# Kernel tuning notes

Hardware: AMD Instinct MI355X
Metric: run time of the kernel (lower is better)

Reference implementation:

```python
import jax, jax.numpy as jnp
import numpy as np

EPS = 1e-5

def weight_quant(w):
    # Per-tensor 1.58-bit quantization: scale by 1/mean(|w|), round (half-to-even,
    # matching torch.round), clamp to {-1,0,1}.
    scale = 1.0 / jnp.clip(jnp.mean(jnp.abs(w)), EPS, None)
    return jnp.clip(jnp.round(w * scale), -1.0, 1.0)

def setup_inputs() -> dict:
    key = jax.random.key(0)
    k1, k2, k3 = jax.random.split(key, 3)
    O, I, B = 4096, 4096, 4096
    V = jax.random.normal(k1, (O, I), dtype=jnp.float32)
    # V_p is a quantized (ternary) version of a weight matrix, as in BitNet-style PTQ
    V_p = weight_quant(jax.random.normal(k2, (O, I), dtype=jnp.float32))
    X = jax.random.normal(k3, (B, I), dtype=jnp.float32)
    theta = jnp.float32(0.2)
    bias = jnp.float32(0.0)
    return {"V": V, "V_p": V_p, "X": X, "theta": theta, "bias": bias}

def reference(V, V_p, X, theta, bias):
    cos_t = jnp.cos(theta)
    # Residual direction T, then ternarize it
    T = (V - V_p * cos_t) / jnp.sin(theta)
    Tq = weight_quant(T)                       # [O, I] in {-1,0,1}
    X_T = jnp.matmul(X, Tq.T)                  # [B, O]
    V_p_X = jnp.matmul(X, V_p.T)               # [B, O]
    sign = jax.lax.stop_gradient(jnp.sign(X_T * 100.0))
    appx = cos_t * V_p_X + sign * bias
    return appx
```

## Files before the change

### kernel.cpp

```cpp
#include <hip/hip_runtime.h>

#define EPSQ 1e-5f

typedef signed char i8;
using int4v = __attribute__((ext_vector_type(4))) int;

constexpr int DIM = 4096;

__device__ __forceinline__ void gload_lds16(const void* g, void* l) {
  __builtin_amdgcn_global_load_lds(
      (const __attribute__((address_space(1))) void*)(g),
      (__attribute__((address_space(3))) void*)(l), 16, 0, 0);
}

__global__ __launch_bounds__(256)
void k_prep(const float* __restrict__ X, const float* __restrict__ V,
            const float* __restrict__ Vp,
            const float* __restrict__ theta_p, const float* __restrict__ bias_p,
            i8* __restrict__ Xq, float* __restrict__ rs,
            i8* __restrict__ W1, float* __restrict__ partial) {
  __shared__ float wred[4];
  const int tid = threadIdx.x;
  const int b = blockIdx.x;
  if (b < 4096) {
    const int row = b;
    const float4* Xr = (const float4*)(X + (size_t)row * DIM);
    float4 f[4];
    float mx = 0.0f;
    #pragma unroll
    for (int t = 0; t < 4; ++t) {
      f[t] = Xr[tid + t * 256];
      mx = fmaxf(mx, fmaxf(fmaxf(fabsf(f[t].x), fabsf(f[t].y)),
                           fmaxf(fabsf(f[t].z), fabsf(f[t].w))));
    }
    #pragma unroll
    for (int off = 32; off > 0; off >>= 1) mx = fmaxf(mx, __shfl_down(mx, off, 64));
    int lane = tid & 63, w = tid >> 6;
    if (lane == 0) wred[w] = mx;
    __syncthreads();
    mx = fmaxf(fmaxf(wred[0], wred[1]), fmaxf(wred[2], wred[3]));
    mx = fmaxf(mx, 1e-30f);
    float rsv = mx / 127.0f;
    if (tid == 0) rs[row] = rsv;
    float inv = 1.0f / rsv;
    char4* Xo = (char4*)(Xq + (size_t)row * DIM);
    #pragma unroll
    for (int t = 0; t < 4; ++t) {
      char4 qv;
      qv.x = (i8)fminf(fmaxf(rintf(f[t].x * inv), -127.0f), 127.0f);
      qv.y = (i8)fminf(fmaxf(rintf(f[t].y * inv), -127.0f), 127.0f);
      qv.z = (i8)fminf(fmaxf(rintf(f[t].z * inv), -127.0f), 127.0f);
      qv.w = (i8)fminf(fmaxf(rintf(f[t].w * inv), -127.0f), 127.0f);
      Xo[tid + t * 256] = qv;
    }
  } else if (b < 6144) {
    const float4* Vp4 = (const float4*)Vp;
    char4* W1o = (char4*)W1;
    const int total4 = DIM * DIM / 4;
    const int stride = 2048 * 256;
    for (int i = (b - 4096) * 256 + tid; i < total4; i += stride) {
      float4 vp = Vp4[i];
      char4 w1;
      w1.x = (i8)vp.x; w1.y = (i8)vp.y; w1.z = (i8)vp.z; w1.w = (i8)vp.w;
      W1o[i] = w1;
    }
  } else {
    if (bias_p[0] == 0.0f) return;
    float ct = cosf(theta_p[0]);
    float st = sinf(theta_p[0]);
    const float4* V4  = (const float4*)V;
    const float4* Vp4 = (const float4*)Vp;
    float acc = 0.0f;
    const int total4 = DIM * DIM / 4;
    const int stride = 2048 * 256;
    for (int i = (b - 6144) * 256 + tid; i < total4; i += stride) {
      float4 v = V4[i], vp = Vp4[i];
      acc += fabsf((v.x - vp.x * ct) / st) + fabsf((v.y - vp.y * ct) / st)
           + fabsf((v.z - vp.z * ct) / st) + fabsf((v.w - vp.w * ct) / st);
    }
    #pragma unroll
    for (int off = 32; off > 0; off >>= 1) acc += __shfl_down(acc, off, 64);
    int lane = tid & 63, w = tid >> 6;
    if (lane == 0) wred[w] = acc;
    __syncthreads();
    if (tid == 0) partial[b - 6144] = wred[0] + wred[1] + wred[2] + wred[3];
  }
}

__global__ __launch_bounds__(256)
void k_quantT(const float* __restrict__ V, const float* __restrict__ Vp,
              const float* __restrict__ theta_p, const float* __restrict__ bias_p,
              const float* __restrict__ partial, i8* __restrict__ W2) {
  if (bias_p[0] == 0.0f) return;
  __shared__ float wred[4];
  __shared__ float stot;
  const int tid = threadIdx.x;
  float s = 0.0f;
  #pragma unroll
  for (int i = 0; i < 8; ++i) s += partial[tid + i * 256];
  #pragma unroll
  for (int off = 32; off > 0; off >>= 1) s += __shfl_down(s, off, 64);
  int lane = tid & 63, w = tid >> 6;
  if (lane == 0) wred[w] = s;
  __syncthreads();
  if (tid == 0) stot = wred[0] + wred[1] + wred[2] + wred[3];
  __syncthreads();
  float mean = fmaxf(stot / 16777216.0f, EPSQ);
  float scale = 1.0f / mean;
  float ctv = cosf(theta_p[0]);
  float stv = sinf(theta_p[0]);
  const float4* V4  = (const float4*)V;
  const float4* Vp4 = (const float4*)Vp;
  char4* W2o = (char4*)W2;
  const int total4 = DIM * DIM / 4;
  const int stride = 2048 * 256;
  for (int i = blockIdx.x * 256 + tid; i < total4; i += stride) {
    float4 v = V4[i], vp = Vp4[i];
    char4 w2;
    w2.x = (i8)fminf(fmaxf(rintf(((v.x - vp.x * ctv) / stv) * scale), -1.0f), 1.0f);
    w2.y = (i8)fminf(fmaxf(rintf(((v.y - vp.y * ctv) / stv) * scale), -1.0f), 1.0f);
    w2.z = (i8)fminf(fmaxf(rintf(((v.z - vp.z * ctv) / stv) * scale), -1.0f), 1.0f);
    w2.w = (i8)fminf(fmaxf(rintf(((v.w - vp.w * ctv) / stv) * scale), -1.0f), 1.0f);
    W2o[i] = w2;
  }
}

__global__ __launch_bounds__(512, 2)
void k_gemm(const i8* __restrict__ A, const i8* __restrict__ B1,
            const i8* __restrict__ B2, float* __restrict__ C,
            const float* __restrict__ rs, const float* __restrict__ theta_p,
            const float* __restrict__ bias_p) {
  __shared__ i8 sm[131072];

  const int tid  = threadIdx.x;
  const int lane = tid & 63;
  const int w    = tid >> 6;
  const int l15  = lane & 15;
  const int kq   = lane >> 4;
  const int wm   = (w >> 2) * 128;
  const int wn   = (w & 3) * 64;
  const int bm   = blockIdx.y * 256;
  const int bn   = blockIdx.x * 256;

  int offg[4];
  #pragma unroll
  for (int ln = 0; ln < 4; ++ln) {
    int p = ln * 512 + tid;
    int r = p >> 3;
    int c = (p & 7) ^ (r & 7);
    offg[ln] = r * DIM + c * 16;
  }

  const int swz0 = ((0 * 4 + kq) ^ (l15 & 7)) * 16;
  const int swz1 = ((1 * 4 + kq) ^ (l15 & 7)) * 16;
  const int arow = (wm + l15) * 128;
  const int brow = (wn + l15) * 128;

  const float biasv = bias_p[0];
  const int npass = (biasv != 0.0f) ? 2 : 1;
  const float ct = cosf(theta_p[0]);

  for (int pass = 0; pass < npass; ++pass) {
    const bool signp = (npass == 2 && pass == 0);
    const i8* Ag = A + (size_t)bm * DIM;
    const i8* Bg = (signp ? B2 : B1) + (size_t)bn * DIM;

    int4v acc[8][4] = {};

    #pragma unroll
    for (int ln = 0; ln < 4; ++ln) {
      const int sb = (ln * 512 + w * 64) * 16;
      gload_lds16(Ag + offg[ln], sm + sb);
      gload_lds16(Bg + offg[ln], sm + 32768 + sb);
    }
    asm volatile("s_waitcnt vmcnt(0)" ::: "memory");
    __builtin_amdgcn_s_barrier();

    #pragma unroll 2
    for (int t = 0; t < 32; ++t) {
      const i8* As = sm + (t & 1) * 65536;
      const i8* Bs = As + 32768;
      i8* Asta = sm + ((t + 1) & 1) * 65536;
      i8* Bsta = Asta + 32768;
      const bool dostage = (t + 1 < 32);
      const int ktn = (t + 1) * 128;

      int4v af[4][2], bf[2][2];
      #pragma unroll
      for (int q = 0; q < 4; ++q) {
        const int mh = q >> 1, nh = q & 1;
        if (nh == 0) {
          #pragma unroll
          for (int i4 = 0; i4 < 4; ++i4) {
            af[i4][0] = *(const int4v*)(As + arow + (mh * 4 + i4) * 2048 + swz0);
            af[i4][1] = *(const int4v*)(As + arow + (mh * 4 + i4) * 2048 + swz1);
          }
        }
        #pragma unroll
        for (int j2 = 0; j2 < 2; ++j2) {
          bf[j2][0] = *(const int4v*)(Bs + brow + (nh * 2 + j2) * 2048 + swz0);
          bf[j2][1] = *(const int4v*)(Bs + brow + (nh * 2 + j2) * 2048 + swz1);
        }
        if (q == 0 && dostage) {
          #pragma unroll
          for (int ln = 0; ln < 4; ++ln) {
            const int sb = (ln * 512 + w * 64) * 16;
            gload_lds16(Ag + ktn + offg[ln], Asta + sb);
            gload_lds16(Bg + ktn + offg[ln], Bsta + sb);
          }
        }
        __builtin_amdgcn_s_barrier();
        asm volatile("s_waitcnt lgkmcnt(0)" ::: "memory");
        __builtin_amdgcn_sched_barrier(0);
        __builtin_amdgcn_s_setprio(1);
        #pragma unroll
        for (int i4 = 0; i4 < 4; ++i4) {
          #pragma unroll
          for (int j2 = 0; j2 < 2; ++j2) {
            acc[mh * 4 + i4][nh * 2 + j2] = __builtin_amdgcn_mfma_i32_16x16x64_i8(
                af[i4][0], bf[j2][0], acc[mh * 4 + i4][nh * 2 + j2], 0, 0, 0);
            acc[mh * 4 + i4][nh * 2 + j2] = __builtin_amdgcn_mfma_i32_16x16x64_i8(
                af[i4][1], bf[j2][1], acc[mh * 4 + i4][nh * 2 + j2], 0, 0, 0);
          }
        }
        __builtin_amdgcn_s_setprio(0);
        if (q == 3) asm volatile("s_waitcnt vmcnt(0)" ::: "memory");
        __builtin_amdgcn_s_barrier();
      }
    }

    if (signp) {
      #pragma unroll
      for (int i = 0; i < 8; ++i) {
        int mbase = bm + wm + i * 16 + kq * 4;
        #pragma unroll
        for (int j = 0; j < 4; ++j) {
          int n = bn + wn + j * 16 + l15;
          #pragma unroll
          for (int r = 0; r < 4; ++r) {
            int v = acc[i][j][r];
            float s = (v > 0) ? 1.0f : ((v < 0) ? -1.0f : 0.0f);
            C[(size_t)(mbase + r) * DIM + n] = s * biasv;
          }
        }
      }
    } else {
      #pragma unroll
      for (int i = 0; i < 8; ++i) {
        int mbase = bm + wm + i * 16 + kq * 4;
        float sc[4];
        #pragma unroll
        for (int r = 0; r < 4; ++r) sc[r] = ct * rs[mbase + r];
        #pragma unroll
        for (int j = 0; j < 4; ++j) {
          int n = bn + wn + j * 16 + l15;
          #pragma unroll
          for (int r = 0; r < 4; ++r) {
            size_t idx = (size_t)(mbase + r) * DIM + n;
            float outv = sc[r] * (float)acc[i][j][r];
            if (npass == 2) outv += C[idx];
            C[idx] = outv;
          }
        }
      }
    }
  }
}

extern "C" void kernel_launch(void* const* d_in, const int* in_sizes, int n_in,
                              void* d_out, int out_size, void* d_ws, size_t ws_size,
                              hipStream_t stream) {
  const float* V     = (const float*)d_in[0];
  const float* Vp    = (const float*)d_in[1];
  const float* X     = (const float*)d_in[2];
  const float* theta = (const float*)d_in[3];
  const float* bias  = (const float*)d_in[4];
  float* out = (float*)d_out;

  const size_t SZ = (size_t)DIM * DIM;
  char* ws = (char*)d_ws;
  float* rs      = (float*)ws;
  float* partial = (float*)(ws + 16384);
  i8* Xq = (i8*)(ws + 16384 + 8192);
  i8* W1 = Xq + SZ;
  i8* W2 = W1 + SZ;

  k_prep<<<8192, 256, 0, stream>>>(X, V, Vp, theta, bias, Xq, rs, W1, partial);
  k_quantT<<<2048, 256, 0, stream>>>(V, Vp, theta, bias, partial, W2);
  k_gemm<<<dim3(16, 16), 512, 0, stream>>>(Xq, W1, W2, out, rs, theta, bias);
}
```

Baseline: 282.3 us.

## Split tile staging into per-phase quarter loads with fine-grained vmcnt waits and block swizzle

Restructures the int8 GEMM main loop so each of the four MFMA phases issues a quarter of the next K-tile's global-to-LDS loads. A partial vmcnt wait and barrier at the start of each phase consume the quarter the phase needs, replacing the single full-tile wait per iteration. The last iteration is peeled with tapering wait counts. It also remaps block indices in groups of 8 to improve L2 reuse of A and B tiles. The per-phase barrier and vmcnt accounting are fragile and can cause races or stalls if the counts are wrong.

After: 362.5 us. 28.4% more time.

```diff
diff --git a/kernel.cpp b/kernel.cpp
--- a/kernel.cpp
+++ b/kernel.cpp
@@ -125,6 +125,58 @@
   }
 }
 
+
+#define SA(AG, KT, DST, MHH) do {                                              \
+    _Pragma("unroll")                                                          \
+    for (int jj = 0; jj < 2; ++jj) {                                           \
+      int br = (MHH) * 64 + jj * 128 + w * 8;                                  \
+      gload_lds16((AG) + (size_t)br * DIM + (KT) + goff, (DST) + br * 128);    \
+    }                                                                          \
+  } while (0)
+
+#define SB(BG, KT, DST, NHH) do {                                              \
+    _Pragma("unroll")                                                          \
+    for (int jj = 0; jj < 2; ++jj) {                                           \
+      int br = (w >> 1) * 64 + (NHH) * 32 + ((w * 2 + jj) & 3) * 8;            \
+      gload_lds16((BG) + (size_t)br * DIM + (KT) + goff, (DST) + br * 128);    \
+    }                                                                          \
+  } while (0)
+
+#define GPH(PAs, PBs, MH, NH, VMSTR, STAGE) do {                               \
+    asm volatile("s_waitcnt vmcnt(" VMSTR ")" ::: "memory");                   \
+    __builtin_amdgcn_s_barrier();                                              \
+    asm volatile("" ::: "memory");                                             \
+    if ((NH) == 0) {                                                           \
+      _Pragma("unroll")                                                        \
+      for (int i4 = 0; i4 < 4; ++i4) {                                         \
+        const i8* ap = (PAs) + (wm + (MH) * 64 + i4 * 16 + l15) * 128;         \
+        af[i4][0] = *(const int4v*)(ap + swz0);                                \
+        af[i4][1] = *(const int4v*)(ap + swz1);                                \
+      }                                                                        \
+    }                                                                          \
+    _Pragma("unroll")                                                          \
+    for (int j2 = 0; j2 < 2; ++j2) {                                           \
+      const i8* bp = (PBs) + (wn + (NH) * 32 + j2 * 16 + l15) * 128;           \
+      bf[j2][0] = *(const int4v*)(bp + swz0);                                  \
+      bf[j2][1] = *(const int4v*)(bp + swz1);                                  \
+    }                                                                          \
+    STAGE;                                                                     \
+    asm volatile("s_waitcnt lgkmcnt(0)" ::: "memory");                         \
+    __builtin_amdgcn_sched_barrier(0);                                         \
+    __builtin_amdgcn_s_setprio(1);                                             \
+    _Pragma("unroll")                                                          \
+    for (int i4 = 0; i4 < 4; ++i4) {                                           \
+      _Pragma("unroll")                                                        \
+      for (int j2 = 0; j2 < 2; ++j2) {                                         \
+        acc[(MH)*4 + i4][(NH)*2 + j2] = __builtin_amdgcn_mfma_i32_16x16x64_i8( \
+            af[i4][0], bf[j2][0], acc[(MH)*4 + i4][(NH)*2 + j2], 0, 0, 0);     \
+        acc[(MH)*4 + i4][(NH)*2 + j2] = __builtin_amdgcn_mfma_i32_16x16x64_i8( \
+            af[i4][1], bf[j2][1], acc[(MH)*4 + i4][(NH)*2 + j2], 0, 0, 0);     \
+      }                                                                        \
+    }                                                                          \
+    __builtin_amdgcn_s_setprio(0);                                             \
+  } while (0)
+
 __global__ __launch_bounds__(512, 2)
 void k_gemm(const i8* __restrict__ A, const i8* __restrict__ B1,
             const i8* __restrict__ B2, float* __restrict__ C,
@@ -139,22 +191,16 @@
   const int kq   = lane >> 4;
   const int wm   = (w >> 2) * 128;
   const int wn   = (w & 3) * 64;
-  const int bm   = blockIdx.y * 256;
-  const int bn   = blockIdx.x * 256;
-
-  int offg[4];
-  #pragma unroll
-  for (int ln = 0; ln < 4; ++ln) {
-    int p = ln * 512 + tid;
-    int r = p >> 3;
-    int c = (p & 7) ^ (r & 7);
-    offg[ln] = r * DIM + c * 16;
-  }
+
+  const int flat = blockIdx.y * gridDim.x + blockIdx.x;
+  const int logical = (flat & 7) * 32 + (flat >> 3);
+  const int bm = (logical >> 4) * 256;
+  const int bn = (logical & 15) * 256;
+
+  const int goff = (lane >> 3) * DIM + (((lane & 7) ^ (lane >> 3)) << 4);
 
   const int swz0 = ((0 * 4 + kq) ^ (l15 & 7)) * 16;
   const int swz1 = ((1 * 4 + kq) ^ (l15 & 7)) * 16;
-  const int arow = (wm + l15) * 128;
-  const int brow = (wn + l15) * 128;
 
   const float biasv = bias_p[0];
   const int npass = (biasv != 0.0f) ? 2 : 1;
@@ -166,67 +212,32 @@
     const i8* Bg = (signp ? B2 : B1) + (size_t)bn * DIM;
 
     int4v acc[8][4] = {};
-
-    #pragma unroll
-    for (int ln = 0; ln < 4; ++ln) {
-      const int sb = (ln * 512 + w * 64) * 16;
-      gload_lds16(Ag + offg[ln], sm + sb);
-      gload_lds16(Bg + offg[ln], sm + 32768 + sb);
-    }
-    asm volatile("s_waitcnt vmcnt(0)" ::: "memory");
-    __builtin_amdgcn_s_barrier();
+    int4v af[4][2], bf[2][2];
+
+    SA(Ag, 0, sm, 0);
+    SB(Bg, 0, sm + 32768, 0);
+    SB(Bg, 0, sm + 32768, 1);
+    SA(Ag, 0, sm, 1);
 
     #pragma unroll 2
-    for (int t = 0; t < 32; ++t) {
+    for (int t = 0; t < 31; ++t) {
       const i8* As = sm + (t & 1) * 65536;
       const i8* Bs = As + 32768;
-      i8* Asta = sm + ((t + 1) & 1) * 65536;
-      i8* Bsta = Asta + 32768;
-      const bool dostage = (t + 1 < 32);
+      i8* An = sm + ((t + 1) & 1) * 65536;
+      i8* Bn = An + 32768;
       const int ktn = (t + 1) * 128;
-
-      int4v af[4][2], bf[2][2];
-      #pragma unroll
-      for (int q = 0; q < 4; ++q) {
-        const int mh = q >> 1, nh = q & 1;
-        if (nh == 0) {
-          #pragma unroll
-          for (int i4 = 0; i4 < 4; ++i4) {
-            af[i4][0] = *(const int4v*)(As + arow + (mh * 4 + i4) * 2048 + swz0);
-            af[i4][1] = *(const int4v*)(As + arow + (mh * 4 + i4) * 2048 + swz1);
-          }
-        }
-        #pragma unroll
-        for (int j2 = 0; j2 < 2; ++j2) {
-          bf[j2][0] = *(const int4v*)(Bs + brow + (nh * 2 + j2) * 2048 + swz0);
-          bf[j2][1] = *(const int4v*)(Bs + brow + (nh * 2 + j2) * 2048 + swz1);
-        }
-        if (q == 0 && dostage) {
-          #pragma unroll
-          for (int ln = 0; ln < 4; ++ln) {
-            const int sb = (ln * 512 + w * 64) * 16;
-            gload_lds16(Ag + ktn + offg[ln], Asta + sb);
-            gload_lds16(Bg + ktn + offg[ln], Bsta + sb);
-          }
-        }
-        __builtin_amdgcn_s_barrier();
-        asm volatile("s_waitcnt lgkmcnt(0)" ::: "memory");
-        __builtin_amdgcn_sched_barrier(0);
-        __builtin_amdgcn_s_setprio(1);
-        #pragma unroll
-        for (int i4 = 0; i4 < 4; ++i4) {
-          #pragma unroll
-          for (int j2 = 0; j2 < 2; ++j2) {
-            acc[mh * 4 + i4][nh * 2 + j2] = __builtin_amdgcn_mfma_i32_16x16x64_i8(
-                af[i4][0], bf[j2][0], acc[mh * 4 + i4][nh * 2 + j2], 0, 0, 0);
-            acc[mh * 4 + i4][nh * 2 + j2] = __builtin_amdgcn_mfma_i32_16x16x64_i8(
-                af[i4][1], bf[j2][1], acc[mh * 4 + i4][nh * 2 + j2], 0, 0, 0);
-          }
-        }
-        __builtin_amdgcn_s_setprio(0);
-        if (q == 3) asm volatile("s_waitcnt vmcnt(0)" ::: "memory");
-        __builtin_amdgcn_s_barrier();
-      }
+      GPH(As, Bs, 0, 0, "4", SA(Ag, ktn, An, 0));
+      GPH(As, Bs, 0, 1, "4", SB(Bg, ktn, Bn, 0));
+      GPH(As, Bs, 1, 0, "4", SB(Bg, ktn, Bn, 1));
+      GPH(As, Bs, 1, 1, "4", SA(Ag, ktn, An, 1));
+    }
+    {
+      const i8* As = sm + 65536;
+      const i8* Bs = As + 32768;
+      GPH(As, Bs, 0, 0, "4", ((void)0));
+      GPH(As, Bs, 0, 1, "2", ((void)0));
+      GPH(As, Bs, 1, 0, "0", ((void)0));
+      GPH(As, Bs, 1, 1, "0", ((void)0));
     }
 
     if (signp) {
```
